# Kernel optimization log

Measured on AMD Instinct MI355X. Metric: run time of the kernel, lower is better.

Reference implementation:

```python
import jax, jax.numpy as jnp
import numpy as np

N = 50000
E = 800000
D = 64


def _linear_params(key, d, bias=True):
    kw, kb = jax.random.split(key)
    s = 1.0 / np.sqrt(d)
    W = jax.random.uniform(kw, (d, d), jnp.float32, -s, s)
    if bias:
        b = jax.random.uniform(kb, (d,), jnp.float32, -s, s)
        return W, b
    return W


def setup_inputs() -> dict:
    key = jax.random.key(0)
    ks = jax.random.split(key, 12)
    x_src = jax.random.normal(ks[0], (N, D), jnp.float32)
    x_tgt = jax.random.normal(ks[1], (N, D), jnp.float32)
    t_src = jax.random.normal(ks[2], (N, D), jnp.float32)
    t_tgt = jax.random.normal(ks[3], (N, D), jnp.float32)
    edge_index = jax.random.randint(ks[4], (2, E), 0, N, jnp.int64)
    W_x = _linear_params(ks[5], D, bias=False)
    W_t = _linear_params(ks[6], D, bias=False)
    Ka_W, Ka_b = _linear_params(ks[7], D)
    Qa_W, Qa_b = _linear_params(ks[8], D)
    Kb_W, Kb_b = _linear_params(ks[9], D)
    Qb_W, Qb_b = _linear_params(ks[10], D)
    return dict(x_src=x_src, x_tgt=x_tgt, t_src=t_src, t_tgt=t_tgt,
                edge_index=edge_index, W_x=W_x, W_t=W_t,
                Ka_W=Ka_W, Ka_b=Ka_b, Qa_W=Qa_W, Qa_b=Qa_b,
                Kb_W=Kb_W, Kb_b=Kb_b, Qb_W=Qb_W, Qb_b=Qb_b)


def _segment_softmax(scores, seg, num_segments):
    # numerically stable softmax over edges sharing the same destination node
    m = jax.ops.segment_max(scores, seg, num_segments=num_segments)
    ex = jnp.exp(scores - m[seg])
    denom = jax.ops.segment_sum(ex, seg, num_segments=num_segments)
    return ex / denom[seg]


def reference(x_src, x_tgt, t_src, t_tgt, edge_index,
              W_x, W_t, Ka_W, Ka_b, Qa_W, Qa_b, Kb_W, Kb_b, Qb_W, Qb_b):
    row, col = edge_index[0], edge_index[1]
    n = x_tgt.shape[0]
    d = x_src.shape[-1]
    scale = 1.0 / jnp.sqrt(jnp.float32(d))

    # project on nodes first (cheaper than per-edge), then gather per edge
    q_alpha = (t_tgt @ Qa_W.T + Qa_b)[row]   # [E, D]
    k_alpha = (t_src @ Ka_W.T + Ka_b)[col]
    alpha = _segment_softmax(jnp.sum(q_alpha * k_alpha, -1) * scale, row, n)

    q_beta = (x_tgt @ Qb_W.T + Qb_b)[row]
    k_beta = (x_src @ Kb_W.T + Kb_b)[col]
    beta = _segment_softmax(jnp.sum(q_beta * k_beta, -1) * scale, row, n)

    msg_t = alpha[:, None] * (t_src @ W_t.T)[col]  # [E, D]
    msg_x = beta[:, None] * (x_src @ W_x.T)[col]

    out_x = jax.ops.segment_sum(msg_x, row, num_segments=n)
    out_t = jax.ops.segment_sum(msg_t, row, num_segments=n)
    return out_x, out_t
```

## Files before the change

kernel.cpp:

```cpp
#include <hip/hip_runtime.h>
#include <math.h>


#define D 64
#define CAP 96
#define NINF -3.0e38f
typedef unsigned short ushortT;
typedef unsigned long long ull;

typedef __attribute__((ext_vector_type(8))) short bf16x8;
typedef __attribute__((ext_vector_type(4))) float f32x4;

__device__ __forceinline__ float b2f(ushortT h) {
  return __uint_as_float(((unsigned)h) << 16);
}
__device__ __forceinline__ float b2f_lo(unsigned u) {
  return __uint_as_float(u << 16);
}
__device__ __forceinline__ float b2f_hi(unsigned u) {
  return __uint_as_float(u & 0xffff0000u);
}
__device__ __forceinline__ ushortT f2b(float f) {
  unsigned u = __float_as_uint(f);
  u += 0x7fffu + ((u >> 16) & 1u);
  return (ushortT)(u >> 16);
}

__device__ __forceinline__ bool wave_is64(const ull* __restrict__ ei, ull nNodes) {
  ull v = ei[threadIdx.x & 63];
  return __ballot(v >= nNodes) == 0ull;
}

__global__ void edge_rank(const void* __restrict__ ei, int* __restrict__ deg,
                          int* __restrict__ rank, int E, ull nNodes) {
  const bool is64 = wave_is64((const ull*)ei, nNodes);
  int base = (blockIdx.x * blockDim.x + threadIdx.x) << 2;
  if (base >= E) return;
  int m = E - base; if (m > 4) m = 4;
  if (is64) {
    const long long* p = (const long long*)ei;
    for (int j = 0; j < m; ++j) {
      int r = (int)p[base + j];
      rank[base + j] = atomicAdd(&deg[r], 1);
    }
  } else {
    const int* p = (const int*)ei;
    for (int j = 0; j < m; ++j) {
      int r = p[base + j];
      rank[base + j] = atomicAdd(&deg[r], 1);
    }
  }
}

__global__ void scan_block_sums(const int* __restrict__ deg, int* __restrict__ bsum, int N) {
  __shared__ int sdata[256];
  int i = blockIdx.x * 256 + threadIdx.x;
  sdata[threadIdx.x] = (i < N) ? deg[i] : 0;
  __syncthreads();
  for (int s = 128; s > 0; s >>= 1) {
    if (threadIdx.x < s) sdata[threadIdx.x] += sdata[threadIdx.x + s];
    __syncthreads();
  }
  if (threadIdx.x == 0) bsum[blockIdx.x] = sdata[0];
}

__global__ void scan_exclusive_small(int* __restrict__ bsum, int nB) {
  __shared__ int sdata[256];
  int t = threadIdx.x;
  int v = (t < nB) ? bsum[t] : 0;
  sdata[t] = v;
  __syncthreads();
  for (int off = 1; off < 256; off <<= 1) {
    int add = (t >= off) ? sdata[t - off] : 0;
    __syncthreads();
    sdata[t] += add;
    __syncthreads();
  }
  if (t < nB) bsum[t] = sdata[t] - v;
}

__global__ void scan_finalize(const int* __restrict__ deg, const int* __restrict__ bsum,
                              int* __restrict__ offs, int N, int E) {
  __shared__ int sdata[256];
  int t = threadIdx.x;
  int i = blockIdx.x * 256 + t;
  int v = (i < N) ? deg[i] : 0;
  sdata[t] = v;
  __syncthreads();
  for (int off = 1; off < 256; off <<= 1) {
    int add = (t >= off) ? sdata[t - off] : 0;
    __syncthreads();
    sdata[t] += add;
    __syncthreads();
  }
  int excl = sdata[t] - v + bsum[blockIdx.x];
  if (i < N) offs[i] = excl;
  if (blockIdx.x == 0 && t == 0) offs[N] = E;
}

__global__ void scatter_edges(const void* __restrict__ ei, const int* __restrict__ offs,
                              const int* __restrict__ rank, int* __restrict__ ecol,
                              int E, ull nNodes) {
  const bool is64 = wave_is64((const ull*)ei, nNodes);
  int base = (blockIdx.x * blockDim.x + threadIdx.x) << 2;
  if (base >= E) return;
  int m = E - base; if (m > 4) m = 4;
  if (is64) {
    const long long* p = (const long long*)ei;
    for (int j = 0; j < m; ++j) {
      int r = (int)p[base + j];
      int c = (int)p[(long long)E + base + j];
      ecol[offs[r] + rank[base + j]] = c;
    }
  } else {
    const int* p = (const int*)ei;
    for (int j = 0; j < m; ++j) {
      int r = p[base + j];
      int c = p[E + base + j];
      ecol[offs[r] + rank[base + j]] = c;
    }
  }
}

#define AROW 72

__global__ __launch_bounds__(256) void proj_mfma(
    const float* __restrict__ t_tgt, const float* __restrict__ x_tgt,
    const float* __restrict__ t_src, const float* __restrict__ x_src,
    const float* __restrict__ QaW, const float* __restrict__ Qab_,
    const float* __restrict__ QbW, const float* __restrict__ Qbb,
    const float* __restrict__ KaW, const float* __restrict__ Kab_,
    const float* __restrict__ Wt,
    const float* __restrict__ KbW, const float* __restrict__ Kbb,
    const float* __restrict__ Wx,
    float* __restrict__ qab, ushortT* __restrict__ kab, ushortT* __restrict__ vtx,
    int nNodes, int bpj) {
  __shared__ ushortT As[128 * AROW];
  __shared__ ushortT W0s[64 * AROW];
  __shared__ ushortT W1s[64 * AROW];
  const int job = blockIdx.x / bpj;
  const int jb = blockIdx.x % bpj;
  const float *X, *W0, *B0, *W1 = nullptr;
  switch (job) {
    case 0: X = t_tgt; W0 = QaW; B0 = Qab_; break;
    case 1: X = x_tgt; W0 = QbW; B0 = Qbb; break;
    case 2: X = t_src; W0 = KaW; B0 = Kab_; W1 = Wt; break;
    default: X = x_src; W0 = KbW; B0 = Kbb; W1 = Wx; break;
  }
  const bool dual = (job >= 2);
  const int half = (job & 1) ? 64 : 0;
  const int tid = threadIdx.x;
  const int base = jb * 128;

#pragma unroll
  for (int r = 0; r < 8; ++r) {
    int idx = tid + 256 * r;
    int row = idx >> 4, k4 = idx & 15;
    int gnode = base + row;
    float4 v = make_float4(0.f, 0.f, 0.f, 0.f);
    if (gnode < nNodes) v = *(const float4*)(X + (size_t)gnode * D + k4 * 4);
    ushort4 h;
    h.x = f2b(v.x); h.y = f2b(v.y); h.z = f2b(v.z); h.w = f2b(v.w);
    *(ushort4*)&As[row * AROW + k4 * 4] = h;
  }
#pragma unroll
  for (int r = 0; r < 4; ++r) {
    int idx = tid + 256 * r;
    int row = idx >> 4, k4 = idx & 15;
    float4 v = *(const float4*)(W0 + row * D + k4 * 4);
    ushort4 h;
    h.x = f2b(v.x); h.y = f2b(v.y); h.z = f2b(v.z); h.w = f2b(v.w);
    *(ushort4*)&W0s[row * AROW + k4 * 4] = h;
  }
  if (dual) {
#pragma unroll
    for (int r = 0; r < 4; ++r) {
      int idx = tid + 256 * r;
      int row = idx >> 4, k4 = idx & 15;
      float4 v = *(const float4*)(W1 + row * D + k4 * 4);
      ushort4 h;
      h.x = f2b(v.x); h.y = f2b(v.y); h.z = f2b(v.z); h.w = f2b(v.w);
      *(ushort4*)&W1s[row * AROW + k4 * 4] = h;
    }
  }
  __syncthreads();

  const int lane = tid & 63;
  const int wid = tid >> 6;
  const int m16 = lane & 15;
  const int quad = lane >> 4;

  f32x4 acc0[2][4], acc1[2][4];
#pragma unroll
  for (int mt = 0; mt < 2; ++mt)
#pragma unroll
    for (int nt = 0; nt < 4; ++nt) {
      acc0[mt][nt] = (f32x4){0.f, 0.f, 0.f, 0.f};
      acc1[mt][nt] = (f32x4){0.f, 0.f, 0.f, 0.f};
    }

#pragma unroll
  for (int ko = 0; ko < 2; ++ko) {
    const int koff = ko * 32 + quad * 8;
    bf16x8 a[2];
#pragma unroll
    for (int mt = 0; mt < 2; ++mt)
      a[mt] = *(const bf16x8*)&As[(wid * 32 + mt * 16 + m16) * AROW + koff];
#pragma unroll
    for (int nt = 0; nt < 4; ++nt) {
      bf16x8 b = *(const bf16x8*)&W0s[(nt * 16 + m16) * AROW + koff];
#pragma unroll
      for (int mt = 0; mt < 2; ++mt)
        acc0[mt][nt] = __builtin_amdgcn_mfma_f32_16x16x32_bf16(
            a[mt], b, acc0[mt][nt], 0, 0, 0);
    }
    if (dual) {
#pragma unroll
      for (int nt = 0; nt < 4; ++nt) {
        bf16x8 b = *(const bf16x8*)&W1s[(nt * 16 + m16) * AROW + koff];
#pragma unroll
        for (int mt = 0; mt < 2; ++mt)
          acc1[mt][nt] = __builtin_amdgcn_mfma_f32_16x16x32_bf16(
              a[mt], b, acc1[mt][nt], 0, 0, 0);
      }
    }
  }

  float bias[4];
#pragma unroll
  for (int nt = 0; nt < 4; ++nt) bias[nt] = B0[nt * 16 + m16];
#pragma unroll
  for (int mt = 0; mt < 2; ++mt) {
#pragma unroll
    for (int reg = 0; reg < 4; ++reg) {
      int node = base + wid * 32 + mt * 16 + quad * 4 + reg;
      if (node < nNodes) {
        if (!dual) {
          float* dst = qab + (size_t)node * 128 + half;
#pragma unroll
          for (int nt = 0; nt < 4; ++nt)
            dst[nt * 16 + m16] = acc0[mt][nt][reg] + bias[nt];
        } else {
          ushortT* dk = kab + (size_t)node * 128 + half;
          ushortT* dv = vtx + (size_t)node * 128 + half;
#pragma unroll
          for (int nt = 0; nt < 4; ++nt) {
            dk[nt * 16 + m16] = f2b(acc0[mt][nt][reg] + bias[nt]);
            dv[nt * 16 + m16] = f2b(acc1[mt][nt][reg]);
          }
        }
      }
    }
  }
}

__global__ __launch_bounds__(256) void node_attn(
    const float* __restrict__ qab, const ushortT* __restrict__ kab,
    const ushortT* __restrict__ vtx,
    const int* __restrict__ offs, const int* __restrict__ ecol,
    float* __restrict__ out_x, float* __restrict__ out_t, int nNodes) {
  __shared__ float s_wa[4][CAP];
  __shared__ float s_wb[4][CAP];
  __shared__ int s_c[4][CAP];
  const int lane = threadIdx.x & 63;
  const int wid = threadIdx.x >> 6;
  const int sub = lane >> 4;
  const int sl = lane & 15;
  const int gw = (blockIdx.x * blockDim.x + threadIdx.x) >> 6;
  const int nw = (gridDim.x * blockDim.x) >> 6;
  const float scale = 0.125f;

  for (int n = gw; n < nNodes; n += nw) {
    const int s = offs[n], e = offs[n + 1], deg = e - s;
    const size_t nb = (size_t)n * D;
    if (deg == 0) {
      out_x[nb + lane] = 0.f;
      out_t[nb + lane] = 0.f;
      continue;
    }
    float acc_t = 0.f, acc_x = 0.f;
    if (deg <= CAP) {
      const float4 q0 = *(const float4*)(qab + (size_t)n * 128 + sl * 8);
      const float4 q1 = *(const float4*)(qab + (size_t)n * 128 + sl * 8 + 4);
      for (int i = 0; i < deg; i += 4) {
        const int idx = i + sub;
        const bool act = idx < deg;
        const int c = ecol[s + (act ? idx : 0)];
        const uint4 u = *(const uint4*)(kab + (size_t)c * 128 + sl * 8);
        float v = q0.x * b2f_lo(u.x);
        v = fmaf(q0.y, b2f_hi(u.x), v);
        v = fmaf(q0.z, b2f_lo(u.y), v);
        v = fmaf(q0.w, b2f_hi(u.y), v);
        v = fmaf(q1.x, b2f_lo(u.z), v);
        v = fmaf(q1.y, b2f_hi(u.z), v);
        v = fmaf(q1.z, b2f_lo(u.w), v);
        v = fmaf(q1.w, b2f_hi(u.w), v);
#pragma unroll
        for (int off = 1; off < 8; off <<= 1) v += __shfl_xor(v, off);
        if (act) {
          if (sl == 0) { s_wa[wid][idx] = v * scale; s_c[wid][idx] = c; }
          if (sl == 8) s_wb[wid][idx] = v * scale;
        }
      }
      float sa = (lane < deg) ? s_wa[wid][lane] : NINF;
      float sb = (lane < deg) ? s_wb[wid][lane] : NINF;
      float ma, mb, da, db;
      if (deg <= 64) {
        ma = sa; mb = sb;
#pragma unroll
        for (int off = 1; off < 64; off <<= 1) {
          ma = fmaxf(ma, __shfl_xor(ma, off));
          mb = fmaxf(mb, __shfl_xor(mb, off));
        }
        float ea = __expf(sa - ma), eb = __expf(sb - mb);
        da = ea; db = eb;
#pragma unroll
        for (int off = 1; off < 64; off <<= 1) {
          da += __shfl_xor(da, off);
          db += __shfl_xor(db, off);
        }
        const float ia = 1.0f / da, ib = 1.0f / db;
        if (lane < deg) { s_wa[wid][lane] = ea * ia; s_wb[wid][lane] = eb * ib; }
      } else {
        float sa1 = (lane + 64 < deg) ? s_wa[wid][lane + 64] : NINF;
        float sb1 = (lane + 64 < deg) ? s_wb[wid][lane + 64] : NINF;
        ma = fmaxf(sa, sa1); mb = fmaxf(sb, sb1);
#pragma unroll
        for (int off = 1; off < 64; off <<= 1) {
          ma = fmaxf(ma, __shfl_xor(ma, off));
          mb = fmaxf(mb, __shfl_xor(mb, off));
        }
        float ea0 = __expf(sa - ma), ea1 = __expf(sa1 - ma);
        float eb0 = __expf(sb - mb), eb1 = __expf(sb1 - mb);
        da = ea0 + ea1; db = eb0 + eb1;
#pragma unroll
        for (int off = 1; off < 64; off <<= 1) {
          da += __shfl_xor(da, off);
          db += __shfl_xor(db, off);
        }
        const float ia = 1.0f / da, ib = 1.0f / db;
        if (lane < deg) { s_wa[wid][lane] = ea0 * ia; s_wb[wid][lane] = eb0 * ib; }
        if (lane + 64 < deg) { s_wa[wid][lane + 64] = ea1 * ia; s_wb[wid][lane + 64] = eb1 * ib; }
      }
      int i = 0;
      for (; i + 2 <= deg; i += 2) {
        const int c0 = s_c[wid][i], c1 = s_c[wid][i + 1];
        const ushortT* b0 = vtx + (size_t)c0 * 128;
        const ushortT* b1 = vtx + (size_t)c1 * 128;
        float t0 = b2f(b0[lane]), x0 = b2f(b0[lane + 64]);
        float t1 = b2f(b1[lane]), x1 = b2f(b1[lane + 64]);
        float wa0 = s_wa[wid][i], wa1 = s_wa[wid][i + 1];
        float wb0 = s_wb[wid][i], wb1 = s_wb[wid][i + 1];
        acc_t = fmaf(wa0, t0, acc_t);
        acc_t = fmaf(wa1, t1, acc_t);
        acc_x = fmaf(wb0, x0, acc_x);
        acc_x = fmaf(wb1, x1, acc_x);
      }
      if (i < deg) {
        const int c0 = s_c[wid][i];
        const ushortT* b0 = vtx + (size_t)c0 * 128;
        acc_t = fmaf(s_wa[wid][i], b2f(b0[lane]), acc_t);
        acc_x = fmaf(s_wb[wid][i], b2f(b0[lane + 64]), acc_x);
      }
    } else {
      const float qla = qab[(size_t)n * 128 + lane];
      const float qlb = qab[(size_t)n * 128 + 64 + lane];
      float ma = NINF, mb = NINF, da = 0.f, db = 0.f;
      for (int i = s; i < e; ++i) {
        int c = ecol[i];
        float va = qla * b2f(kab[(size_t)c * 128 + lane]);
        float vb = qlb * b2f(kab[(size_t)c * 128 + 64 + lane]);
#pragma unroll
        for (int off = 1; off < 64; off <<= 1) {
          va += __shfl_xor(va, off);
          vb += __shfl_xor(vb, off);
        }
        va *= scale; vb *= scale;
        float na = fmaxf(ma, va);
        da = da * __expf(ma - na) + __expf(va - na);
        ma = na;
        float nb2 = fmaxf(mb, vb);
        db = db * __expf(mb - nb2) + __expf(vb - nb2);
        mb = nb2;
      }
      const float ia = 1.0f / da, ib = 1.0f / db;
      for (int i = s; i < e; ++i) {
        int c = ecol[i];
        float va = qla * b2f(kab[(size_t)c * 128 + lane]);
        float vb = qlb * b2f(kab[(size_t)c * 128 + 64 + lane]);
#pragma unroll
        for (int off = 1; off < 64; off <<= 1) {
          va += __shfl_xor(va, off);
          vb += __shfl_xor(vb, off);
        }
        float al = __expf(va * scale - ma) * ia;
        float be = __expf(vb * scale - mb) * ib;
        const ushortT* b0 = vtx + (size_t)c * 128;
        acc_t = fmaf(al, b2f(b0[lane]), acc_t);
        acc_x = fmaf(be, b2f(b0[lane + 64]), acc_x);
      }
    }
    out_t[nb + lane] = acc_t;
    out_x[nb + lane] = acc_x;
  }
}

extern "C" void kernel_launch(void* const* d_in, const int* in_sizes, int n_in,
                              void* d_out, int out_size, void* d_ws, size_t ws_size,
                              hipStream_t stream) {
  const float* x_src = (const float*)d_in[0];
  const float* x_tgt = (const float*)d_in[1];
  const float* t_src = (const float*)d_in[2];
  const float* t_tgt = (const float*)d_in[3];
  const void* edge_index = d_in[4];
  const float* W_x = (const float*)d_in[5];
  const float* W_t = (const float*)d_in[6];
  const float* Ka_W = (const float*)d_in[7];
  const float* Ka_b = (const float*)d_in[8];
  const float* Qa_W = (const float*)d_in[9];
  const float* Qa_b = (const float*)d_in[10];
  const float* Kb_W = (const float*)d_in[11];
  const float* Kb_b = (const float*)d_in[12];
  const float* Qb_W = (const float*)d_in[13];
  const float* Qb_b = (const float*)d_in[14];

  const int N = in_sizes[0] / D;
  const int E = in_sizes[4] / 2;
  const int nB = (N + 255) / 256;

  char* ws = (char*)d_ws;
  size_t ofs = 0;
  auto carve = [&](size_t bytes) {
    size_t p = ofs;
    ofs += (bytes + 255) & ~(size_t)255;
    return p;
  };
  float* qab = (float*)(ws + carve((size_t)N * 128 * 4));
  ushortT* kab = (ushortT*)(ws + carve((size_t)N * 128 * 2));
  ushortT* vtx = (ushortT*)(ws + carve((size_t)N * 128 * 2));
  int* offs = (int*)(ws + carve(((size_t)N + 1) * 4));
  int* deg = (int*)(ws + carve((size_t)N * 4));
  int* bsum = (int*)(ws + carve((size_t)nB * 4));
  int* rank = (int*)(ws + carve((size_t)E * 4));
  int* ecol = (int*)(ws + carve((size_t)E * 4));
  (void)ws_size;

  float* out_x = (float*)d_out;
  float* out_t = out_x + (size_t)N * D;

  const int e4Blocks = ((E + 3) / 4 + 255) / 256;

  hipMemsetAsync(deg, 0, (size_t)N * 4, stream);
  edge_rank<<<e4Blocks, 256, 0, stream>>>(edge_index, deg, rank, E, (ull)N);
  scan_block_sums<<<nB, 256, 0, stream>>>(deg, bsum, N);
  scan_exclusive_small<<<1, 256, 0, stream>>>(bsum, nB);
  scan_finalize<<<nB, 256, 0, stream>>>(deg, bsum, offs, N, E);
  scatter_edges<<<e4Blocks, 256, 0, stream>>>(edge_index, offs, rank, ecol, E, (ull)N);

  const int bpj = (N + 127) / 128;
  proj_mfma<<<4 * bpj, 256, 0, stream>>>(t_tgt, x_tgt, t_src, x_src,
                                         Qa_W, Qa_b, Qb_W, Qb_b,
                                         Ka_W, Ka_b, W_t,
                                         Kb_W, Kb_b, W_x,
                                         qab, kab, vtx, N, bpj);

  node_attn<<<(N + 3) / 4, 256, 0, stream>>>(qab, kab, vtx, offs, ecol,
                                             out_x, out_t, N);
}
```

Baseline: 267.1 us.

## Fuse CSR build and projections into one persistent kernel; stage neighbor values in LDS

New measurement: 632.2 us. +136.7%, slower.

```diff
diff --git a/kernel.cpp b/kernel.cpp
--- a/kernel.cpp
+++ b/kernel.cpp
@@ -4,10 +4,13 @@
 
 #define D 64
 #define CAP 96
+#define PC 24
 #define NINF -3.0e38f
+#define GRID_PRE 512
+#define MAGIC 0x4D416743
+#define AROW 72
 typedef unsigned short ushortT;
 typedef unsigned long long ull;
-
 typedef __attribute__((ext_vector_type(8))) short bf16x8;
 typedef __attribute__((ext_vector_type(4))) float f32x4;
 
@@ -31,100 +34,28 @@
   return __ballot(v >= nNodes) == 0ull;
 }
 
-__global__ void edge_rank(const void* __restrict__ ei, int* __restrict__ deg,
-                          int* __restrict__ rank, int E, ull nNodes) {
-  const bool is64 = wave_is64((const ull*)ei, nNodes);
-  int base = (blockIdx.x * blockDim.x + threadIdx.x) << 2;
-  if (base >= E) return;
-  int m = E - base; if (m > 4) m = 4;
-  if (is64) {
-    const long long* p = (const long long*)ei;
-    for (int j = 0; j < m; ++j) {
-      int r = (int)p[base + j];
-      rank[base + j] = atomicAdd(&deg[r], 1);
-    }
-  } else {
-    const int* p = (const int*)ei;
-    for (int j = 0; j < m; ++j) {
-      int r = p[base + j];
-      rank[base + j] = atomicAdd(&deg[r], 1);
-    }
-  }
-}
-
-__global__ void scan_block_sums(const int* __restrict__ deg, int* __restrict__ bsum, int N) {
-  __shared__ int sdata[256];
-  int i = blockIdx.x * 256 + threadIdx.x;
-  sdata[threadIdx.x] = (i < N) ? deg[i] : 0;
+__device__ __forceinline__ void gbar(int* cnt, int* gen) {
   __syncthreads();
-  for (int s = 128; s > 0; s >>= 1) {
-    if (threadIdx.x < s) sdata[threadIdx.x] += sdata[threadIdx.x + s];
-    __syncthreads();
-  }
-  if (threadIdx.x == 0) bsum[blockIdx.x] = sdata[0];
-}
-
-__global__ void scan_exclusive_small(int* __restrict__ bsum, int nB) {
-  __shared__ int sdata[256];
-  int t = threadIdx.x;
-  int v = (t < nB) ? bsum[t] : 0;
-  sdata[t] = v;
+  if (threadIdx.x == 0) {
+    int g = __hip_atomic_load(gen, __ATOMIC_RELAXED, __HIP_MEMORY_SCOPE_AGENT);
+    __threadfence();
+    int prev = __hip_atomic_fetch_add(cnt, 1, __ATOMIC_ACQ_REL,
+                                      __HIP_MEMORY_SCOPE_AGENT);
+    if (prev == GRID_PRE - 1) {
+      __hip_atomic_store(cnt, 0, __ATOMIC_RELAXED, __HIP_MEMORY_SCOPE_AGENT);
+      __threadfence();
+      __hip_atomic_fetch_add(gen, 1, __ATOMIC_ACQ_REL, __HIP_MEMORY_SCOPE_AGENT);
+    } else {
+      while (__hip_atomic_load(gen, __ATOMIC_ACQUIRE,
+                               __HIP_MEMORY_SCOPE_AGENT) == g)
+        __builtin_amdgcn_s_sleep(2);
+    }
+    __threadfence();
+  }
   __syncthreads();
-  for (int off = 1; off < 256; off <<= 1) {
-    int add = (t >= off) ? sdata[t - off] : 0;
-    __syncthreads();
-    sdata[t] += add;
-    __syncthreads();
-  }
-  if (t < nB) bsum[t] = sdata[t] - v;
-}
-
-__global__ void scan_finalize(const int* __restrict__ deg, const int* __restrict__ bsum,
-                              int* __restrict__ offs, int N, int E) {
-  __shared__ int sdata[256];
-  int t = threadIdx.x;
-  int i = blockIdx.x * 256 + t;
-  int v = (i < N) ? deg[i] : 0;
-  sdata[t] = v;
-  __syncthreads();
-  for (int off = 1; off < 256; off <<= 1) {
-    int add = (t >= off) ? sdata[t - off] : 0;
-    __syncthreads();
-    sdata[t] += add;
-    __syncthreads();
-  }
-  int excl = sdata[t] - v + bsum[blockIdx.x];
-  if (i < N) offs[i] = excl;
-  if (blockIdx.x == 0 && t == 0) offs[N] = E;
-}
-
-__global__ void scatter_edges(const void* __restrict__ ei, const int* __restrict__ offs,
-                              const int* __restrict__ rank, int* __restrict__ ecol,
-                              int E, ull nNodes) {
-  const bool is64 = wave_is64((const ull*)ei, nNodes);
-  int base = (blockIdx.x * blockDim.x + threadIdx.x) << 2;
-  if (base >= E) return;
-  int m = E - base; if (m > 4) m = 4;
-  if (is64) {
-    const long long* p = (const long long*)ei;
-    for (int j = 0; j < m; ++j) {
-      int r = (int)p[base + j];
-      int c = (int)p[(long long)E + base + j];
-      ecol[offs[r] + rank[base + j]] = c;
-    }
-  } else {
-    const int* p = (const int*)ei;
-    for (int j = 0; j < m; ++j) {
-      int r = p[base + j];
-      int c = p[E + base + j];
-      ecol[offs[r] + rank[base + j]] = c;
-    }
-  }
-}
-
-#define AROW 72
-
-__global__ __launch_bounds__(256) void proj_mfma(
+}
+
+__global__ __launch_bounds__(256, 3) void fused_pre(
     const float* __restrict__ t_tgt, const float* __restrict__ x_tgt,
     const float* __restrict__ t_src, const float* __restrict__ x_src,
     const float* __restrict__ QaW, const float* __restrict__ Qab_,
@@ -134,120 +65,235 @@
     const float* __restrict__ KbW, const float* __restrict__ Kbb,
     const float* __restrict__ Wx,
     float* __restrict__ qab, ushortT* __restrict__ kab, ushortT* __restrict__ vtx,
-    int nNodes, int bpj) {
+    const void* __restrict__ ei, int E, int N, int bpj,
+    int* __restrict__ deg, int* __restrict__ rank, int* __restrict__ offs,
+    int* __restrict__ ecol, int* __restrict__ bsum, int* __restrict__ bar) {
   __shared__ ushortT As[128 * AROW];
   __shared__ ushortT W0s[64 * AROW];
   __shared__ ushortT W1s[64 * AROW];
-  const int job = blockIdx.x / bpj;
-  const int jb = blockIdx.x % bpj;
-  const float *X, *W0, *B0, *W1 = nullptr;
-  switch (job) {
-    case 0: X = t_tgt; W0 = QaW; B0 = Qab_; break;
-    case 1: X = x_tgt; W0 = QbW; B0 = Qbb; break;
-    case 2: X = t_src; W0 = KaW; B0 = Kab_; W1 = Wt; break;
-    default: X = x_src; W0 = KbW; B0 = Kbb; W1 = Wx; break;
-  }
-  const bool dual = (job >= 2);
-  const int half = (job & 1) ? 64 : 0;
   const int tid = threadIdx.x;
-  const int base = jb * 128;
-
-#pragma unroll
-  for (int r = 0; r < 8; ++r) {
-    int idx = tid + 256 * r;
-    int row = idx >> 4, k4 = idx & 15;
-    int gnode = base + row;
-    float4 v = make_float4(0.f, 0.f, 0.f, 0.f);
-    if (gnode < nNodes) v = *(const float4*)(X + (size_t)gnode * D + k4 * 4);
-    ushort4 h;
-    h.x = f2b(v.x); h.y = f2b(v.y); h.z = f2b(v.z); h.w = f2b(v.w);
-    *(ushort4*)&As[row * AROW + k4 * 4] = h;
-  }
-#pragma unroll
-  for (int r = 0; r < 4; ++r) {
-    int idx = tid + 256 * r;
-    int row = idx >> 4, k4 = idx & 15;
-    float4 v = *(const float4*)(W0 + row * D + k4 * 4);
-    ushort4 h;
-    h.x = f2b(v.x); h.y = f2b(v.y); h.z = f2b(v.z); h.w = f2b(v.w);
-    *(ushort4*)&W0s[row * AROW + k4 * 4] = h;
-  }
-  if (dual) {
+
+  const int nTiles = 4 * bpj;
+  for (int tile = blockIdx.x; tile < nTiles; tile += GRID_PRE) {
+    __syncthreads();
+    const int job = tile / bpj;
+    const int jb = tile % bpj;
+    const float *X, *W0, *B0, *W1 = nullptr;
+    switch (job) {
+      case 0: X = t_tgt; W0 = QaW; B0 = Qab_; break;
+      case 1: X = x_tgt; W0 = QbW; B0 = Qbb; break;
+      case 2: X = t_src; W0 = KaW; B0 = Kab_; W1 = Wt; break;
+      default: X = x_src; W0 = KbW; B0 = Kbb; W1 = Wx; break;
+    }
+    const bool dual = (job >= 2);
+    const int half = (job & 1) ? 64 : 0;
+    const int base = jb * 128;
+
+#pragma unroll
+    for (int r = 0; r < 8; ++r) {
+      int idx = tid + 256 * r;
+      int row = idx >> 4, k4 = idx & 15;
+      int gnode = base + row;
+      float4 v = make_float4(0.f, 0.f, 0.f, 0.f);
+      if (gnode < N) v = *(const float4*)(X + (size_t)gnode * D + k4 * 4);
+      ushort4 h;
+      h.x = f2b(v.x); h.y = f2b(v.y); h.z = f2b(v.z); h.w = f2b(v.w);
+      *(ushort4*)&As[row * AROW + k4 * 4] = h;
+    }
 #pragma unroll
     for (int r = 0; r < 4; ++r) {
       int idx = tid + 256 * r;
       int row = idx >> 4, k4 = idx & 15;
-      float4 v = *(const float4*)(W1 + row * D + k4 * 4);
+      float4 v = *(const float4*)(W0 + row * D + k4 * 4);
       ushort4 h;
       h.x = f2b(v.x); h.y = f2b(v.y); h.z = f2b(v.z); h.w = f2b(v.w);
-      *(ushort4*)&W1s[row * AROW + k4 * 4] = h;
-    }
+      *(ushort4*)&W0s[row * AROW + k4 * 4] = h;
+    }
+    if (dual) {
+#pragma unroll
+      for (int r = 0; r < 4; ++r) {
+        int idx = tid + 256 * r;
+        int row = idx >> 4, k4 = idx & 15;
+        float4 v = *(const float4*)(W1 + row * D + k4 * 4);
+        ushort4 h;
+        h.x = f2b(v.x); h.y = f2b(v.y); h.z = f2b(v.z); h.w = f2b(v.w);
+        *(ushort4*)&W1s[row * AROW + k4 * 4] = h;
+      }
+    }
+    __syncthreads();
+
+    const int lane = tid & 63;
+    const int wid = tid >> 6;
+    const int m16 = lane & 15;
+    const int quad = lane >> 4;
+
+    f32x4 acc0[2][4], acc1[2][4];
+#pragma unroll
+    for (int mt = 0; mt < 2; ++mt)
+#pragma unroll
+      for (int nt = 0; nt < 4; ++nt) {
+        acc0[mt][nt] = (f32x4){0.f, 0.f, 0.f, 0.f};
+        acc1[mt][nt] = (f32x4){0.f, 0.f, 0.f, 0.f};
+      }
+#pragma unroll
+    for (int ko = 0; ko < 2; ++ko) {
+      const int koff = ko * 32 + quad * 8;
+      bf16x8 a[2];
+#pragma unroll
+      for (int mt = 0; mt < 2; ++mt)
+        a[mt] = *(const bf16x8*)&As[(wid * 32 + mt * 16 + m16) * AROW + koff];
+#pragma unroll
+      for (int nt = 0; nt < 4; ++nt) {
+        bf16x8 b = *(const bf16x8*)&W0s[(nt * 16 + m16) * AROW + koff];
+#pragma unroll
+        for (int mt = 0; mt < 2; ++mt)
+          acc0[mt][nt] = __builtin_amdgcn_mfma_f32_16x16x32_bf16(
+              a[mt], b, acc0[mt][nt], 0, 0, 0);
+      }
+      if (dual) {
+#pragma unroll
+        for (int nt = 0; nt < 4; ++nt) {
+          bf16x8 b = *(const bf16x8*)&W1s[(nt * 16 + m16) * AROW + koff];
+#pragma unroll
+          for (int mt = 0; mt < 2; ++mt)
+            acc1[mt][nt] = __builtin_amdgcn_mfma_f32_16x16x32_bf16(
+                a[mt], b, acc1[mt][nt], 0, 0, 0);
+        }
+      }
+    }
+
+    float bias[4];
+#pragma unroll
+    for (int nt = 0; nt < 4; ++nt) bias[nt] = B0[nt * 16 + m16];
+#pragma unroll
+    for (int mt = 0; mt < 2; ++mt) {
+#pragma unroll
+      for (int reg = 0; reg < 4; ++reg) {
+        int node = base + wid * 32 + mt * 16 + quad * 4 + reg;
+        if (node < N) {
+          if (!dual) {
+            float* dst = qab + (size_t)node * 128 + half;
+#pragma unroll
+            for (int nt = 0; nt < 4; ++nt)
+              dst[nt * 16 + m16] = acc0[mt][nt][reg] + bias[nt];
+          } else {
+            ushortT* dk = kab + (size_t)node * 128 + half;
+            ushortT* dv = vtx + (size_t)node * 128 + half;
+#pragma unroll
+            for (int nt = 0; nt < 4; ++nt) {
+              dk[nt * 16 + m16] = f2b(acc0[mt][nt][reg] + bias[nt]);
+              dv[nt * 16 + m16] = f2b(acc1[mt][nt][reg]);
+            }
+          }
+        }
+      }
+    }
+  }
+
+  if (blockIdx.x == 0 && tid == 0) {
+    bar[1] = 0;
+    bar[2] = 0;
+    __threadfence();
+    __hip_atomic_store(&bar[0], MAGIC, __ATOMIC_RELEASE, __HIP_MEMORY_SCOPE_AGENT);
+  }
+  if (tid == 0) {
+    while (__hip_atomic_load(&bar[0], __ATOMIC_ACQUIRE,
+                             __HIP_MEMORY_SCOPE_AGENT) != MAGIC)
+      __builtin_amdgcn_s_sleep(2);
   }
   __syncthreads();
 
-  const int lane = tid & 63;
-  const int wid = tid >> 6;
-  const int m16 = lane & 15;
-  const int quad = lane >> 4;
-
-  f32x4 acc0[2][4], acc1[2][4];
-#pragma unroll
-  for (int mt = 0; mt < 2; ++mt)
-#pragma unroll
-    for (int nt = 0; nt < 4; ++nt) {
-      acc0[mt][nt] = (f32x4){0.f, 0.f, 0.f, 0.f};
-      acc1[mt][nt] = (f32x4){0.f, 0.f, 0.f, 0.f};
-    }
-
-#pragma unroll
-  for (int ko = 0; ko < 2; ++ko) {
-    const int koff = ko * 32 + quad * 8;
-    bf16x8 a[2];
-#pragma unroll
-    for (int mt = 0; mt < 2; ++mt)
-      a[mt] = *(const bf16x8*)&As[(wid * 32 + mt * 16 + m16) * AROW + koff];
-#pragma unroll
-    for (int nt = 0; nt < 4; ++nt) {
-      bf16x8 b = *(const bf16x8*)&W0s[(nt * 16 + m16) * AROW + koff];
-#pragma unroll
-      for (int mt = 0; mt < 2; ++mt)
-        acc0[mt][nt] = __builtin_amdgcn_mfma_f32_16x16x32_bf16(
-            a[mt], b, acc0[mt][nt], 0, 0, 0);
-    }
-    if (dual) {
-#pragma unroll
-      for (int nt = 0; nt < 4; ++nt) {
-        bf16x8 b = *(const bf16x8*)&W1s[(nt * 16 + m16) * AROW + koff];
-#pragma unroll
-        for (int mt = 0; mt < 2; ++mt)
-          acc1[mt][nt] = __builtin_amdgcn_mfma_f32_16x16x32_bf16(
-              a[mt], b, acc1[mt][nt], 0, 0, 0);
-      }
-    }
-  }
-
-  float bias[4];
-#pragma unroll
-  for (int nt = 0; nt < 4; ++nt) bias[nt] = B0[nt * 16 + m16];
-#pragma unroll
-  for (int mt = 0; mt < 2; ++mt) {
-#pragma unroll
-    for (int reg = 0; reg < 4; ++reg) {
-      int node = base + wid * 32 + mt * 16 + quad * 4 + reg;
-      if (node < nNodes) {
-        if (!dual) {
-          float* dst = qab + (size_t)node * 128 + half;
-#pragma unroll
-          for (int nt = 0; nt < 4; ++nt)
-            dst[nt * 16 + m16] = acc0[mt][nt][reg] + bias[nt];
-        } else {
-          ushortT* dk = kab + (size_t)node * 128 + half;
-          ushortT* dv = vtx + (size_t)node * 128 + half;
-#pragma unroll
-          for (int nt = 0; nt < 4; ++nt) {
-            dk[nt * 16 + m16] = f2b(acc0[mt][nt][reg] + bias[nt]);
-            dv[nt * 16 + m16] = f2b(acc1[mt][nt][reg]);
-          }
+  const int gtid = blockIdx.x * 256 + tid;
+  int* sI = (int*)As;
+
+  for (int i = gtid; i < N; i += GRID_PRE * 256) deg[i] = 0;
+  gbar(&bar[1], &bar[2]);
+
+  {
+    const bool is64 = wave_is64((const ull*)ei, (ull)N);
+    const int stride4 = GRID_PRE * 256 * 4;
+    for (int i4 = gtid * 4; i4 < E; i4 += stride4) {
+      int m = E - i4; if (m > 4) m = 4;
+      if (is64) {
+        const long long* p = (const long long*)ei;
+        for (int j = 0; j < m; ++j) {
+          int r = (int)p[i4 + j];
+          rank[i4 + j] = atomicAdd(&deg[r], 1);
+        }
+      } else {
+        const int* p = (const int*)ei;
+        for (int j = 0; j < m; ++j) {
+          int r = p[i4 + j];
+          rank[i4 + j] = atomicAdd(&deg[r], 1);
+        }
+      }
+    }
+  }
+  gbar(&bar[1], &bar[2]);
+
+  {
+    int n = gtid;
+    int d = (n < N) ? deg[n] : 0;
+    sI[tid] = d;
+    __syncthreads();
+    for (int s = 128; s > 0; s >>= 1) {
+      if (tid < s) sI[tid] += sI[tid + s];
+      __syncthreads();
+    }
+    if (tid == 0) bsum[blockIdx.x] = sI[0];
+  }
+  gbar(&bar[1], &bar[2]);
+
+  if (blockIdx.x == 0) {
+    int v = bsum[tid];
+    sI[tid] = v;
+    __syncthreads();
+    for (int off = 1; off < 256; off <<= 1) {
+      int add = (tid >= off) ? sI[tid - off] : 0;
+      __syncthreads();
+      sI[tid] += add;
+      __syncthreads();
+    }
+    bsum[tid] = sI[tid] - v;
+  }
+  gbar(&bar[1], &bar[2]);
+
+  {
+    int n = gtid;
+    int d = (n < N) ? deg[n] : 0;
+    sI[tid] = d;
+    __syncthreads();
+    for (int off = 1; off < 256; off <<= 1) {
+      int add = (tid >= off) ? sI[tid - off] : 0;
+      __syncthreads();
+      sI[tid] += add;
+      __syncthreads();
+    }
+    if (blockIdx.x < 256 && n <= N) {
+      int excl = sI[tid] - d + bsum[blockIdx.x];
+      offs[n] = excl;
+    }
+  }
+  gbar(&bar[1], &bar[2]);
+
+  {
+    const bool is64 = wave_is64((const ull*)ei, (ull)N);
+    const int stride4 = GRID_PRE * 256 * 4;
+    for (int i4 = gtid * 4; i4 < E; i4 += stride4) {
+      int m = E - i4; if (m > 4) m = 4;
+      if (is64) {
+        const long long* p = (const long long*)ei;
+        for (int j = 0; j < m; ++j) {
+          int r = (int)p[i4 + j];
+          int c = (int)p[(long long)E + i4 + j];
+          ecol[offs[r] + rank[i4 + j]] = c;
+        }
+      } else {
+        const int* p = (const int*)ei;
+        for (int j = 0; j < m; ++j) {
+          int r = p[i4 + j];
+          int c = p[E + i4 + j];
+          ecol[offs[r] + rank[i4 + j]] = c;
         }
       }
     }
@@ -259,6 +305,7 @@
     const ushortT* __restrict__ vtx,
     const int* __restrict__ offs, const int* __restrict__ ecol,
     float* __restrict__ out_x, float* __restrict__ out_t, int nNodes) {
+  __shared__ __align__(16) ushortT s_v[4][PC][136];
   __shared__ float s_wa[4][CAP];
   __shared__ float s_wb[4][CAP];
   __shared__ int s_c[4][CAP];
@@ -287,6 +334,8 @@
         const bool act = idx < deg;
         const int c = ecol[s + (act ? idx : 0)];
         const uint4 u = *(const uint4*)(kab + (size_t)c * 128 + sl * 8);
+        uint4 w = make_uint4(0, 0, 0, 0);
+        if (idx < PC) w = *(const uint4*)(vtx + (size_t)c * 128 + sl * 8);
         float v = q0.x * b2f_lo(u.x);
         v = fmaf(q0.y, b2f_hi(u.x), v);
         v = fmaf(q0.z, b2f_lo(u.y), v);
@@ -297,6 +346,7 @@
         v = fmaf(q1.w, b2f_hi(u.w), v);
 #pragma unroll
         for (int off = 1; off < 8; off <<= 1) v += __shfl_xor(v, off);
+        if (act && idx < PC) *(uint4*)&s_v[wid][idx][sl * 8] = w;
         if (act) {
           if (sl == 0) { s_wa[wid][idx] = v * scale; s_c[wid][idx] = c; }
           if (sl == 8) s_wb[wid][idx] = v * scale;
@@ -304,16 +354,15 @@
       }
       float sa = (lane < deg) ? s_wa[wid][lane] : NINF;
       float sb = (lane < deg) ? s_wb[wid][lane] : NINF;
-      float ma, mb, da, db;
       if (deg <= 64) {
-        ma = sa; mb = sb;
+        float ma = sa, mb = sb;
 #pragma unroll
         for (int off = 1; off < 64; off <<= 1) {
           ma = fmaxf(ma, __shfl_xor(ma, off));
           mb = fmaxf(mb, __shfl_xor(mb, off));
         }
         float ea = __expf(sa - ma), eb = __expf(sb - mb);
-        da = ea; db = eb;
+        float da = ea, db = eb;
 #pragma unroll
         for (int off = 1; off < 64; off <<= 1) {
           da += __shfl_xor(da, off);
@@ -324,7 +373,7 @@
       } else {
         float sa1 = (lane + 64 < deg) ? s_wa[wid][lane + 64] : NINF;
         float sb1 = (lane + 64 < deg) ? s_wb[wid][lane + 64] : NINF;
-        ma = fmaxf(sa, sa1); mb = fmaxf(sb, sb1);
+        float ma = fmaxf(sa, sa1), mb = fmaxf(sb, sb1);
 #pragma unroll
         for (int off = 1; off < 64; off <<= 1) {
           ma = fmaxf(ma, __shfl_xor(ma, off));
@@ -332,7 +381,7 @@
         }
         float ea0 = __expf(sa - ma), ea1 = __expf(sa1 - ma);
         float eb0 = __expf(sb - mb), eb1 = __expf(sb1 - mb);
-        da = ea0 + ea1; db = eb0 + eb1;
+        float da = ea0 + ea1, db = eb0 + eb1;
 #pragma unroll
         for (int off = 1; off < 64; off <<= 1) {
           da += __shfl_xor(da, off);
@@ -340,23 +389,28 @@
         }
         const float ia = 1.0f / da, ib = 1.0f / db;
         if (lane < deg) { s_wa[wid][lane] = ea0 * ia; s_wb[wid][lane] = eb0 * ib; }
-        if (lane + 64 < deg) { s_wa[wid][lane + 64] = ea1 * ia; s_wb[wid][lane + 64] = eb1 * ib; }
-      }
+        if (lane + 64 < deg) {
+          s_wa[wid][lane + 64] = ea1 * ia;
+          s_wb[wid][lane + 64] = eb1 * ib;
+        }
+      }
+      const int lim = deg < PC ? deg : PC;
       int i = 0;
-      for (; i + 2 <= deg; i += 2) {
-        const int c0 = s_c[wid][i], c1 = s_c[wid][i + 1];
-        const ushortT* b0 = vtx + (size_t)c0 * 128;
-        const ushortT* b1 = vtx + (size_t)c1 * 128;
-        float t0 = b2f(b0[lane]), x0 = b2f(b0[lane + 64]);
-        float t1 = b2f(b1[lane]), x1 = b2f(b1[lane + 64]);
-        float wa0 = s_wa[wid][i], wa1 = s_wa[wid][i + 1];
-        float wb0 = s_wb[wid][i], wb1 = s_wb[wid][i + 1];
-        acc_t = fmaf(wa0, t0, acc_t);
-        acc_t = fmaf(wa1, t1, acc_t);
-        acc_x = fmaf(wb0, x0, acc_x);
-        acc_x = fmaf(wb1, x1, acc_x);
-      }
-      if (i < deg) {
+      for (; i + 2 <= lim; i += 2) {
+        float t0 = b2f(s_v[wid][i][lane]);
+        float x0 = b2f(s_v[wid][i][lane + 64]);
+        float t1 = b2f(s_v[wid][i + 1][lane]);
+        float x1 = b2f(s_v[wid][i + 1][lane + 64]);
+        acc_t = fmaf(s_wa[wid][i], t0, acc_t);
+        acc_t = fmaf(s_wa[wid][i + 1], t1, acc_t);
+        acc_x = fmaf(s_wb[wid][i], x0, acc_x);
+        acc_x = fmaf(s_wb[wid][i + 1], x1, acc_x);
+      }
+      for (; i < lim; ++i) {
+        acc_t = fmaf(s_wa[wid][i], b2f(s_v[wid][i][lane]), acc_t);
+        acc_x = fmaf(s_wb[wid][i], b2f(s_v[wid][i][lane + 64]), acc_x);
+      }
+      for (; i < deg; ++i) {
         const int c0 = s_c[wid][i];
         const ushortT* b0 = vtx + (size_t)c0 * 128;
         acc_t = fmaf(s_wa[wid][i], b2f(b0[lane]), acc_t);
@@ -426,7 +480,6 @@
 
   const int N = in_sizes[0] / D;
   const int E = in_sizes[4] / 2;
-  const int nB = (N + 255) / 256;
 
   char* ws = (char*)d_ws;
   size_t ofs = 0;
@@ -440,29 +493,25 @@
   ushortT* vtx = (ushortT*)(ws + carve((size_t)N * 128 * 2));
   int* offs = (int*)(ws + carve(((size_t)N + 1) * 4));
   int* deg = (int*)(ws + carve((size_t)N * 4));
-  int* bsum = (int*)(ws + carve((size_t)nB * 4));
   int* rank = (int*)(ws + carve((size_t)E * 4));
   int* ecol = (int*)(ws + carve((size_t)E * 4));
+  int* bsum = (int*)(ws + carve((size_t)GRID_PRE * 4));
+  int* bar = (int*)(ws + carve(64));
   (void)ws_size;
 
   float* out_x = (float*)d_out;
   float* out_t = out_x + (size_t)N * D;
 
-  const int e4Blocks = ((E + 3) / 4 + 255) / 256;
-
-  hipMemsetAsync(deg, 0, (size_t)N * 4, stream);
-  edge_rank<<<e4Blocks, 256, 0, stream>>>(edge_index, deg, rank, E, (ull)N);
-  scan_block_sums<<<nB, 256, 0, stream>>>(deg, bsum, N);
-  scan_exclusive_small<<<1, 256, 0, stream>>>(bsum, nB);
-  scan_finalize<<<nB, 256, 0, stream>>>(deg, bsum, offs, N, E);
-  scatter_edges<<<e4Blocks, 256, 0, stream>>>(edge_index, offs, rank, ecol, E, (ull)N);
-
   const int bpj = (N + 127) / 128;
-  proj_mfma<<<4 * bpj, 256, 0, stream>>>(t_tgt, x_tgt, t_src, x_src,
-                                         Qa_W, Qa_b, Qb_W, Qb_b,
-                                         Ka_W, Ka_b, W_t,
-                                         Kb_W, Kb_b, W_x,
-                                         qab, kab, vtx, N, bpj);
+
+  fused_pre<<<GRID_PRE, 256, 0, stream>>>(
+      t_tgt, x_tgt, t_src, x_src,
+      Qa_W, Qa_b, Qb_W, Qb_b,
+      Ka_W, Ka_b, W_t,
+      Kb_W, Kb_b, W_x,
+      qab, kab, vtx,
+      edge_index, E, N, bpj,
+      deg, rank, offs, ecol, bsum, bar);
 
   node_attn<<<(N + 3) / 4, 256, 0, stream>>>(qab, kab, vtx, offs, ecol,
                                              out_x, out_t, N);
```

## Fuse scan kernels, merge edge scatter with projection, stage values in LDS

Applied to the files above, without the earlier changes.

Measured after the change: 333.5 us. 1.25x slower.

```diff
diff --git a/kernel.cpp b/kernel.cpp
--- a/kernel.cpp
+++ b/kernel.cpp
@@ -4,10 +4,11 @@
 
 #define D 64
 #define CAP 96
+#define PC 24
 #define NINF -3.0e38f
+#define AROW 72
 typedef unsigned short ushortT;
 typedef unsigned long long ull;
-
 typedef __attribute__((ext_vector_type(8))) short bf16x8;
 typedef __attribute__((ext_vector_type(4))) float f32x4;
 
@@ -52,79 +53,52 @@
   }
 }
 
-__global__ void scan_block_sums(const int* __restrict__ deg, int* __restrict__ bsum, int N) {
-  __shared__ int sdata[256];
-  int i = blockIdx.x * 256 + threadIdx.x;
-  sdata[threadIdx.x] = (i < N) ? deg[i] : 0;
+__global__ __launch_bounds__(1024) void scan_offs(const int* __restrict__ deg,
+                                                  int* __restrict__ offs,
+                                                  int N, int E) {
+  __shared__ int wsum[16];
+  __shared__ int carryS;
+  const int tid = threadIdx.x;
+  const int lane = tid & 63, wv = tid >> 6;
+  if (tid == 0) carryS = 0;
   __syncthreads();
-  for (int s = 128; s > 0; s >>= 1) {
-    if (threadIdx.x < s) sdata[threadIdx.x] += sdata[threadIdx.x + s];
+  int d_next = (tid < N) ? deg[tid] : 0;
+  for (int base = 0; base < N; base += 1024) {
+    const int idx = base + tid;
+    const int d = d_next;
+    const int nidx = base + 1024 + tid;
+    d_next = (nidx < N) ? deg[nidx] : 0;
+    int x = d;
+#pragma unroll
+    for (int off = 1; off < 64; off <<= 1) {
+      int y = __shfl_up(x, off);
+      if (lane >= off) x += y;
+    }
+    if (lane == 63) wsum[wv] = x;
     __syncthreads();
-  }
-  if (threadIdx.x == 0) bsum[blockIdx.x] = sdata[0];
-}
-
-__global__ void scan_exclusive_small(int* __restrict__ bsum, int nB) {
-  __shared__ int sdata[256];
-  int t = threadIdx.x;
-  int v = (t < nB) ? bsum[t] : 0;
-  sdata[t] = v;
-  __syncthreads();
-  for (int off = 1; off < 256; off <<= 1) {
-    int add = (t >= off) ? sdata[t - off] : 0;
+    if (wv == 0) {
+      int s = (lane < 16) ? wsum[lane] : 0;
+#pragma unroll
+      for (int off = 1; off < 16; off <<= 1) {
+        int y = __shfl_up(s, off);
+        if (lane >= off) s += y;
+      }
+      if (lane < 16) wsum[lane] = s;
+    }
     __syncthreads();
-    sdata[t] += add;
+    const int waveOff = (wv > 0) ? wsum[wv - 1] : 0;
+    const int excl = x - d + waveOff + carryS;
+    if (idx < N) offs[idx] = excl;
     __syncthreads();
-  }
-  if (t < nB) bsum[t] = sdata[t] - v;
-}
-
-__global__ void scan_finalize(const int* __restrict__ deg, const int* __restrict__ bsum,
-                              int* __restrict__ offs, int N, int E) {
-  __shared__ int sdata[256];
-  int t = threadIdx.x;
-  int i = blockIdx.x * 256 + t;
-  int v = (i < N) ? deg[i] : 0;
-  sdata[t] = v;
-  __syncthreads();
-  for (int off = 1; off < 256; off <<= 1) {
-    int add = (t >= off) ? sdata[t - off] : 0;
+    if (tid == 0) carryS += wsum[15];
     __syncthreads();
-    sdata[t] += add;
-    __syncthreads();
-  }
-  int excl = sdata[t] - v + bsum[blockIdx.x];
-  if (i < N) offs[i] = excl;
-  if (blockIdx.x == 0 && t == 0) offs[N] = E;
-}
-
-__global__ void scatter_edges(const void* __restrict__ ei, const int* __restrict__ offs,
-                              const int* __restrict__ rank, int* __restrict__ ecol,
-                              int E, ull nNodes) {
-  const bool is64 = wave_is64((const ull*)ei, nNodes);
-  int base = (blockIdx.x * blockDim.x + threadIdx.x) << 2;
-  if (base >= E) return;
-  int m = E - base; if (m > 4) m = 4;
-  if (is64) {
-    const long long* p = (const long long*)ei;
-    for (int j = 0; j < m; ++j) {
-      int r = (int)p[base + j];
-      int c = (int)p[(long long)E + base + j];
-      ecol[offs[r] + rank[base + j]] = c;
-    }
-  } else {
-    const int* p = (const int*)ei;
-    for (int j = 0; j < m; ++j) {
-      int r = p[base + j];
-      int c = p[E + base + j];
-      ecol[offs[r] + rank[base + j]] = c;
-    }
-  }
-}
-
-#define AROW 72
-
-__global__ __launch_bounds__(256) void proj_mfma(
+  }
+  if (tid == 0) offs[N] = E;
+}
+
+__global__ __launch_bounds__(256) void scat_proj(
+    const void* __restrict__ ei, const int* __restrict__ offs,
+    const int* __restrict__ rank, int* __restrict__ ecol, int E,
     const float* __restrict__ t_tgt, const float* __restrict__ x_tgt,
     const float* __restrict__ t_src, const float* __restrict__ x_src,
     const float* __restrict__ QaW, const float* __restrict__ Qab_,
@@ -134,12 +108,38 @@
     const float* __restrict__ KbW, const float* __restrict__ Kbb,
     const float* __restrict__ Wx,
     float* __restrict__ qab, ushortT* __restrict__ kab, ushortT* __restrict__ vtx,
-    int nNodes, int bpj) {
+    int N, int bpj, int scatBlocks) {
   __shared__ ushortT As[128 * AROW];
   __shared__ ushortT W0s[64 * AROW];
   __shared__ ushortT W1s[64 * AROW];
-  const int job = blockIdx.x / bpj;
-  const int jb = blockIdx.x % bpj;
+  const int tid = threadIdx.x;
+
+  if (blockIdx.x < scatBlocks) {
+    const bool is64 = wave_is64((const ull*)ei, (ull)N);
+    int base = (blockIdx.x * 256 + tid) << 2;
+    if (base >= E) return;
+    int m = E - base; if (m > 4) m = 4;
+    if (is64) {
+      const long long* p = (const long long*)ei;
+      for (int j = 0; j < m; ++j) {
+        int r = (int)p[base + j];
+        int c = (int)p[(long long)E + base + j];
+        ecol[offs[r] + rank[base + j]] = c;
+      }
+    } else {
+      const int* p = (const int*)ei;
+      for (int j = 0; j < m; ++j) {
+        int r = p[base + j];
+        int c = p[E + base + j];
+        ecol[offs[r] + rank[base + j]] = c;
+      }
+    }
+    return;
+  }
+
+  const int tile = blockIdx.x - scatBlocks;
+  const int job = tile / bpj;
+  const int jb = tile % bpj;
   const float *X, *W0, *B0, *W1 = nullptr;
   switch (job) {
     case 0: X = t_tgt; W0 = QaW; B0 = Qab_; break;
@@ -149,7 +149,6 @@
   }
   const bool dual = (job >= 2);
   const int half = (job & 1) ? 64 : 0;
-  const int tid = threadIdx.x;
   const int base = jb * 128;
 
 #pragma unroll
@@ -158,7 +157,7 @@
     int row = idx >> 4, k4 = idx & 15;
     int gnode = base + row;
     float4 v = make_float4(0.f, 0.f, 0.f, 0.f);
-    if (gnode < nNodes) v = *(const float4*)(X + (size_t)gnode * D + k4 * 4);
+    if (gnode < N) v = *(const float4*)(X + (size_t)gnode * D + k4 * 4);
     ushort4 h;
     h.x = f2b(v.x); h.y = f2b(v.y); h.z = f2b(v.z); h.w = f2b(v.w);
     *(ushort4*)&As[row * AROW + k4 * 4] = h;
@@ -198,7 +197,6 @@
       acc0[mt][nt] = (f32x4){0.f, 0.f, 0.f, 0.f};
       acc1[mt][nt] = (f32x4){0.f, 0.f, 0.f, 0.f};
     }
-
 #pragma unroll
   for (int ko = 0; ko < 2; ++ko) {
     const int koff = ko * 32 + quad * 8;
@@ -234,7 +232,7 @@
 #pragma unroll
     for (int reg = 0; reg < 4; ++reg) {
       int node = base + wid * 32 + mt * 16 + quad * 4 + reg;
-      if (node < nNodes) {
+      if (node < N) {
         if (!dual) {
           float* dst = qab + (size_t)node * 128 + half;
 #pragma unroll
@@ -259,6 +257,7 @@
     const ushortT* __restrict__ vtx,
     const int* __restrict__ offs, const int* __restrict__ ecol,
     float* __restrict__ out_x, float* __restrict__ out_t, int nNodes) {
+  __shared__ __align__(16) ushortT s_v[4][PC][136];
   __shared__ float s_wa[4][CAP];
   __shared__ float s_wb[4][CAP];
   __shared__ int s_c[4][CAP];
@@ -287,6 +286,8 @@
         const bool act = idx < deg;
         const int c = ecol[s + (act ? idx : 0)];
         const uint4 u = *(const uint4*)(kab + (size_t)c * 128 + sl * 8);
+        uint4 w = make_uint4(0, 0, 0, 0);
+        if (idx < PC) w = *(const uint4*)(vtx + (size_t)c * 128 + sl * 8);
         float v = q0.x * b2f_lo(u.x);
         v = fmaf(q0.y, b2f_hi(u.x), v);
         v = fmaf(q0.z, b2f_lo(u.y), v);
@@ -297,6 +298,7 @@
         v = fmaf(q1.w, b2f_hi(u.w), v);
 #pragma unroll
         for (int off = 1; off < 8; off <<= 1) v += __shfl_xor(v, off);
+        if (act && idx < PC) *(uint4*)&s_v[wid][idx][sl * 8] = w;
         if (act) {
           if (sl == 0) { s_wa[wid][idx] = v * scale; s_c[wid][idx] = c; }
           if (sl == 8) s_wb[wid][idx] = v * scale;
@@ -304,16 +306,15 @@
       }
       float sa = (lane < deg) ? s_wa[wid][lane] : NINF;
       float sb = (lane < deg) ? s_wb[wid][lane] : NINF;
-      float ma, mb, da, db;
       if (deg <= 64) {
-        ma = sa; mb = sb;
+        float ma = sa, mb = sb;
 #pragma unroll
         for (int off = 1; off < 64; off <<= 1) {
           ma = fmaxf(ma, __shfl_xor(ma, off));
           mb = fmaxf(mb, __shfl_xor(mb, off));
         }
         float ea = __expf(sa - ma), eb = __expf(sb - mb);
-        da = ea; db = eb;
+        float da = ea, db = eb;
 #pragma unroll
         for (int off = 1; off < 64; off <<= 1) {
           da += __shfl_xor(da, off);
@@ -324,7 +325,7 @@
       } else {
         float sa1 = (lane + 64 < deg) ? s_wa[wid][lane + 64] : NINF;
         float sb1 = (lane + 64 < deg) ? s_wb[wid][lane + 64] : NINF;
-        ma = fmaxf(sa, sa1); mb = fmaxf(sb, sb1);
+        float ma = fmaxf(sa, sa1), mb = fmaxf(sb, sb1);
 #pragma unroll
         for (int off = 1; off < 64; off <<= 1) {
           ma = fmaxf(ma, __shfl_xor(ma, off));
@@ -332,7 +333,7 @@
         }
         float ea0 = __expf(sa - ma), ea1 = __expf(sa1 - ma);
         float eb0 = __expf(sb - mb), eb1 = __expf(sb1 - mb);
-        da = ea0 + ea1; db = eb0 + eb1;
+        float da = ea0 + ea1, db = eb0 + eb1;
 #pragma unroll
         for (int off = 1; off < 64; off <<= 1) {
           da += __shfl_xor(da, off);
@@ -340,23 +341,28 @@
         }
         const float ia = 1.0f / da, ib = 1.0f / db;
         if (lane < deg) { s_wa[wid][lane] = ea0 * ia; s_wb[wid][lane] = eb0 * ib; }
-        if (lane + 64 < deg) { s_wa[wid][lane + 64] = ea1 * ia; s_wb[wid][lane + 64] = eb1 * ib; }
-      }
+        if (lane + 64 < deg) {
+          s_wa[wid][lane + 64] = ea1 * ia;
+          s_wb[wid][lane + 64] = eb1 * ib;
+        }
+      }
+      const int lim = deg < PC ? deg : PC;
       int i = 0;
-      for (; i + 2 <= deg; i += 2) {
-        const int c0 = s_c[wid][i], c1 = s_c[wid][i + 1];
-        const ushortT* b0 = vtx + (size_t)c0 * 128;
-        const ushortT* b1 = vtx + (size_t)c1 * 128;
-        float t0 = b2f(b0[lane]), x0 = b2f(b0[lane + 64]);
-        float t1 = b2f(b1[lane]), x1 = b2f(b1[lane + 64]);
-        float wa0 = s_wa[wid][i], wa1 = s_wa[wid][i + 1];
-        float wb0 = s_wb[wid][i], wb1 = s_wb[wid][i + 1];
-        acc_t = fmaf(wa0, t0, acc_t);
-        acc_t = fmaf(wa1, t1, acc_t);
-        acc_x = fmaf(wb0, x0, acc_x);
-        acc_x = fmaf(wb1, x1, acc_x);
-      }
-      if (i < deg) {
+      for (; i + 2 <= lim; i += 2) {
+        float t0 = b2f(s_v[wid][i][lane]);
+        float x0 = b2f(s_v[wid][i][lane + 64]);
+        float t1 = b2f(s_v[wid][i + 1][lane]);
+        float x1 = b2f(s_v[wid][i + 1][lane + 64]);
+        acc_t = fmaf(s_wa[wid][i], t0, acc_t);
+        acc_t = fmaf(s_wa[wid][i + 1], t1, acc_t);
+        acc_x = fmaf(s_wb[wid][i], x0, acc_x);
+        acc_x = fmaf(s_wb[wid][i + 1], x1, acc_x);
+      }
+      for (; i < lim; ++i) {
+        acc_t = fmaf(s_wa[wid][i], b2f(s_v[wid][i][lane]), acc_t);
+        acc_x = fmaf(s_wb[wid][i], b2f(s_v[wid][i][lane + 64]), acc_x);
+      }
+      for (; i < deg; ++i) {
         const int c0 = s_c[wid][i];
         const ushortT* b0 = vtx + (size_t)c0 * 128;
         acc_t = fmaf(s_wa[wid][i], b2f(b0[lane]), acc_t);
@@ -426,7 +432,6 @@
 
   const int N = in_sizes[0] / D;
   const int E = in_sizes[4] / 2;
-  const int nB = (N + 255) / 256;
 
   char* ws = (char*)d_ws;
   size_t ofs = 0;
@@ -440,7 +445,6 @@
   ushortT* vtx = (ushortT*)(ws + carve((size_t)N * 128 * 2));
   int* offs = (int*)(ws + carve(((size_t)N + 1) * 4));
   int* deg = (int*)(ws + carve((size_t)N * 4));
-  int* bsum = (int*)(ws + carve((size_t)nB * 4));
   int* rank = (int*)(ws + carve((size_t)E * 4));
   int* ecol = (int*)(ws + carve((size_t)E * 4));
   (void)ws_size;
@@ -448,22 +452,19 @@
   float* out_x = (float*)d_out;
   float* out_t = out_x + (size_t)N * D;
 
-  const int e4Blocks = ((E + 3) / 4 + 255) / 256;
+  const int scatBlocks = ((E + 3) / 4 + 255) / 256;
+  const int bpj = (N + 127) / 128;
 
   hipMemsetAsync(deg, 0, (size_t)N * 4, stream);
-  edge_rank<<<e4Blocks, 256, 0, stream>>>(edge_index, deg, rank, E, (ull)N);
-  scan_block_sums<<<nB, 256, 0, stream>>>(deg, bsum, N);
-  scan_exclusive_small<<<1, 256, 0, stream>>>(bsum, nB);
-  scan_finalize<<<nB, 256, 0, stream>>>(deg, bsum, offs, N, E);
-  scatter_edges<<<e4Blocks, 256, 0, stream>>>(edge_index, offs, rank, ecol, E, (ull)N);
-
-  const int bpj = (N + 127) / 128;
-  proj_mfma<<<4 * bpj, 256, 0, stream>>>(t_tgt, x_tgt, t_src, x_src,
-                                         Qa_W, Qa_b, Qb_W, Qb_b,
-                                         Ka_W, Ka_b, W_t,
-                                         Kb_W, Kb_b, W_x,
-                                         qab, kab, vtx, N, bpj);
-
+  edge_rank<<<scatBlocks, 256, 0, stream>>>(edge_index, deg, rank, E, (ull)N);
+  scan_offs<<<1, 1024, 0, stream>>>(deg, offs, N, E);
+  scat_proj<<<scatBlocks + 4 * bpj, 256, 0, stream>>>(
+      edge_index, offs, rank, ecol, E,
+      t_tgt, x_tgt, t_src, x_src,
+      Qa_W, Qa_b, Qb_W, Qb_b,
+      Ka_W, Ka_b, W_t,
+      Kb_W, Kb_b, W_x,
+      qab, kab, vtx, N, bpj, scatBlocks);
   node_attn<<<(N + 3) / 4, 256, 0, stream>>>(qab, kab, vtx, offs, ecol,
                                              out_x, out_t, N);
 }
```
